# Kernel tuning notes

Hardware: AMD Instinct MI355X
Metric: run time of the kernel (lower is better)

The kernel has to match this reference:

```python
import jax, jax.numpy as jnp
import numpy as np

WD, WH, WW = 1, 8, 8           # window size
NH = 2                          # num heads
EPS = 1e-5                      # torch LayerNorm default


def _layernorm(x, g, b):
    mu = jnp.mean(x, axis=-1, keepdims=True)
    var = jnp.mean((x - mu) ** 2, axis=-1, keepdims=True)
    return (x - mu) * jax.lax.rsqrt(var + EPS) * g + b


def setup_inputs() -> dict:
    key = jax.random.key(0)
    ks = jax.random.split(key, 12)
    C, H = 192, 768  # dim, mlp hidden
    w = lambda k, shape: (jax.random.normal(k, shape, jnp.float32) * 0.02)
    return {
        "x": jax.random.normal(ks[0], (2, 8, 96, 96, C), jnp.float32),
        "norm3_g": jnp.ones((C,), jnp.float32),
        "norm3_b": jnp.zeros((C,), jnp.float32),
        "in_proj_w": w(ks[1], (3 * C, C)),
        "in_proj_b": jnp.zeros((3 * C,), jnp.float32),
        "out_proj_w": w(ks[2], (C, C)),
        "out_proj_b": jnp.zeros((C,), jnp.float32),
        "norm4_g": jnp.ones((C,), jnp.float32),
        "norm4_b": jnp.zeros((C,), jnp.float32),
        "fc1_w": w(ks[3], (H, C)),
        "fc1_b": jnp.zeros((H,), jnp.float32),
        "fc2_w": w(ks[4], (C, H)),
        "fc2_b": jnp.zeros((C,), jnp.float32),
    }


def _part3(x, norm3_g, norm3_b, in_proj_w, in_proj_b, out_proj_w, out_proj_b):
    B, D, H, W, C = x.shape
    Dn, Hn, Wn = D // WD, H // WH, W // WW
    P = Hn * Wn          # spatial windows
    Wt = WD * WH * WW    # tokens per window (64)
    L = Dn * Wt          # attention sequence length

    xn = _layernorm(x, norm3_g, norm3_b)
    # window partition: (B, Dn, Hn, Wn, wd, wh, ww, C)
    xw = xn.reshape(B, Dn, WD, Hn, WH, Wn, WW, C).transpose(0, 1, 3, 5, 2, 4, 6, 7)
    # tgt: (B, Dn, P, Wt, C) -> h: (B*P, Dn*Wt, C)
    tgt = xw.reshape(B, Dn, P, Wt, C)
    h = tgt.transpose(0, 2, 1, 3, 4).reshape(B * P, L, C)

    # qkv projection (torch Linear convention: x @ W.T + b)
    qkv = h @ in_proj_w.T + in_proj_b          # (Bp, L, 3C)
    q, k, v = jnp.split(qkv, 3, axis=-1)
    hd = C // NH
    q = q.reshape(B * P, L, NH, hd)
    k = k.reshape(B * P, L, NH, hd)
    v = v.reshape(B * P, L, NH, hd)

    # block-causal mask over temporal index (each block is Wt x Wt)
    neg_inf = jnp.finfo(jnp.float32).min
    tmask = jnp.triu(jnp.full((Dn, Dn), neg_inf, jnp.float32), k=1)
    mask = jnp.repeat(jnp.repeat(tmask, Wt, axis=0), Wt, axis=1)  # (L, L)

    scale = 1.0 / np.sqrt(hd)
    scores = jnp.einsum("blhd,bmhd->bhlm", q * scale, k) + mask
    attn = jax.nn.softmax(scores, axis=-1)
    out = jnp.einsum("bhlm,bmhd->blhd", attn, v).reshape(B * P, L, C)
    out = out @ out_proj_w.T + out_proj_b

    # reverse: (B, P, Dn, Wt, C) -> windows -> (B, D, H, W, C)
    out = out.reshape(B, P, Dn, Wt, C).transpose(0, 2, 1, 3, 4)
    out = out.reshape(B, Dn, Hn, Wn, WD, WH, WW, C)
    out = out.transpose(0, 1, 4, 2, 5, 3, 6, 7).reshape(B, D, H, W, C)
    return out


def reference(x, norm3_g, norm3_b, in_proj_w, in_proj_b, out_proj_w, out_proj_b,
              norm4_g, norm4_b, fc1_w, fc1_b, fc2_w, fc2_b):
    x = x + _part3(x, norm3_g, norm3_b, in_proj_w, in_proj_b, out_proj_w, out_proj_b)
    xn = _layernorm(x, norm4_g, norm4_b)
    mlp = jax.nn.gelu(xn @ fc1_w.T + fc1_b, approximate=False) @ fc2_w.T + fc2_b
    return x + mlp
```

## Files before the change

### kernel.cpp

```cpp
#include <hip/hip_runtime.h>
#include <cstdint>
#include <cstddef>


typedef float   f32x4  __attribute__((ext_vector_type(4)));
typedef __bf16  bf16x8 __attribute__((ext_vector_type(8)));
typedef unsigned int   u32x4  __attribute__((ext_vector_type(4)));
typedef unsigned short u16x4  __attribute__((ext_vector_type(4)));

#define DEVI __device__ __forceinline__

DEVI float bf2f(unsigned short u) {
    union { unsigned int i; float f; } v; v.i = ((unsigned int)u) << 16; return v.f;
}
DEVI unsigned short f2bf(float f) {
    unsigned int u = __builtin_bit_cast(unsigned int, f);
    unsigned int r = u + 0x7fffu + ((u >> 16) & 1u);
    return (unsigned short)(r >> 16);
}

typedef __attribute__((address_space(3))) unsigned char       lds_u8;
typedef __attribute__((address_space(1))) const unsigned char g_u8;
DEVI void gl_lds16(const void* g, void* l) {
    __builtin_amdgcn_global_load_lds((g_u8*)g, (lds_u8*)l, 16, 0, 0);
}

__global__ __launch_bounds__(256) void k_wconv(const float* __restrict__ wqkv,
                                               const float* __restrict__ wout,
                                               const float* __restrict__ wfc1,
                                               const float* __restrict__ wfc2,
                                               unsigned short* __restrict__ oq,
                                               unsigned short* __restrict__ oo,
                                               unsigned short* __restrict__ o1,
                                               unsigned short* __restrict__ o2) {
    int i = blockIdx.x * 256 + threadIdx.x;
    if (i < 122880) {
        int r = i / 192;
        oq[i] = (r < 576) ? f2bf(wqkv[i]) : (unsigned short)0;
    } else if (i < 172032) {
        int j = i - 122880; int r = j / 192;
        oo[j] = (r < 192) ? f2bf(wout[j]) : (unsigned short)0;
    } else if (i < 319488) {
        int j = i - 172032;
        o1[j] = f2bf(wfc1[j]);
    } else if (i < 516096) {
        int j = i - 319488; int r = j / 768;
        o2[j] = (r < 192) ? f2bf(wfc2[j]) : (unsigned short)0;
    }
}

__global__ __launch_bounds__(256) void k_ln3(const float* __restrict__ x,
                                             const float* __restrict__ g,
                                             const float* __restrict__ bsh,
                                             unsigned short* __restrict__ h) {
    int w = threadIdx.x >> 6, lane = threadIdx.x & 63;
    int token = blockIdx.x * 4 + w;
    const float* xp = x + (size_t)token * 192;
    float v0 = xp[lane], v1 = xp[lane + 64], v2 = xp[lane + 128];
    float s = v0 + v1 + v2;
#pragma unroll
    for (int off = 32; off; off >>= 1) s += __shfl_xor(s, off);
    float mean = s * (1.f / 192.f);
    float d0 = v0 - mean, d1 = v1 - mean, d2 = v2 - mean;
    float q = d0 * d0 + d1 * d1 + d2 * d2;
#pragma unroll
    for (int off = 32; off; off >>= 1) q += __shfl_xor(q, off);
    float rs = rsqrtf(q * (1.f / 192.f) + 1e-5f);
    int b  = token / (8 * 96 * 96);
    int r0 = token - b * (8 * 96 * 96);
    int d  = r0 / (96 * 96);
    int r1 = r0 - d * (96 * 96);
    int hh = r1 / 96;
    int ww = r1 - hh * 96;
    int bp = b * 144 + (hh >> 3) * 12 + (ww >> 3);
    int l  = d * 64 + (hh & 7) * 8 + (ww & 7);
    unsigned short* hp = h + ((size_t)bp * 512 + l) * 192;
    hp[lane]       = f2bf(d0 * rs * g[lane]       + bsh[lane]);
    hp[lane + 64]  = f2bf(d1 * rs * g[lane + 64]  + bsh[lane + 64]);
    hp[lane + 128] = f2bf(d2 * rs * g[lane + 128] + bsh[lane + 128]);
}

__global__ __launch_bounds__(256) void k_ln4b(const unsigned short* __restrict__ yb,
                                              const float* __restrict__ g,
                                              const float* __restrict__ bsh,
                                              unsigned short* __restrict__ xn) {
    int sub = threadIdx.x >> 5, tl = threadIdx.x & 31;
    size_t row = (size_t)blockIdx.x * 8 + sub;
    const unsigned int* rp = reinterpret_cast<const unsigned int*>(yb + row * 192);
    float v[6];
#pragma unroll
    for (int j = 0; j < 3; j++) {
        unsigned int w = rp[tl + 32 * j];
        v[2 * j]     = bf2f((unsigned short)(w & 0xffffu));
        v[2 * j + 1] = bf2f((unsigned short)(w >> 16));
    }
    float s = v[0] + v[1] + v[2] + v[3] + v[4] + v[5];
#pragma unroll
    for (int off = 1; off < 32; off <<= 1) s += __shfl_xor(s, off);
    float mean = s * (1.f / 192.f);
    float q = 0.f;
#pragma unroll
    for (int j = 0; j < 6; j++) { v[j] -= mean; q += v[j] * v[j]; }
#pragma unroll
    for (int off = 1; off < 32; off <<= 1) q += __shfl_xor(q, off);
    float rs = rsqrtf(q * (1.f / 192.f) + 1e-5f);
    unsigned int* op = reinterpret_cast<unsigned int*>(xn + row * 192);
#pragma unroll
    for (int j = 0; j < 3; j++) {
        int c = (tl + 32 * j) * 2;
        unsigned short lo = f2bf(v[2 * j]     * rs * g[c]     + bsh[c]);
        unsigned short hi = f2bf(v[2 * j + 1] * rs * g[c + 1] + bsh[c + 1]);
        op[tl + 32 * j] = ((unsigned int)hi << 16) | lo;
    }
}

template <int EPI, int K>
__global__ __launch_bounds__(256) void k_gemm128(const unsigned short* __restrict__ A,
                                                 const unsigned short* __restrict__ Bw,
                                                 const float* __restrict__ bias,
                                                 unsigned short* __restrict__ outb,
                                                 unsigned short* __restrict__ vt,
                                                 float* __restrict__ outf,
                                                 const float* __restrict__ res,
                                                 const unsigned short* __restrict__ resb) {
    __shared__ unsigned short As[2][128 * 64];
    __shared__ unsigned short Bs[2][128 * 64];
    const int tid = threadIdx.x;
    const int nwg = gridDim.x * gridDim.y;
    const int flat = blockIdx.y * gridDim.x + blockIdx.x;
    const int swz = (flat & 7) * (nwg >> 3) + (flat >> 3);
    const int bx = swz % gridDim.x, by = swz / gridDim.x;
    const int row0 = by * 128, col0 = bx * 128;
    const int wv = tid >> 6, lane = tid & 63, lr = lane & 15, lg = lane >> 4;
    const int wr = wv >> 1, wc = wv & 1;
    const int sr = lane >> 3, sc = lane & 7;
    f32x4 acc[4][4] = {};

    auto stage = [&](int t, int buf) {
        int k0 = t * 64;
#pragma unroll
        for (int i = 0; i < 4; i++) {
            int gq = wv * 4 + i;
            int r = gq * 8 + sr;
            int j = sc ^ (r & 7);
            gl_lds16(A + (size_t)(row0 + r) * K + k0 + j * 8, &As[buf][gq * 512]);
        }
#pragma unroll
        for (int i = 0; i < 4; i++) {
            int gq = wv * 4 + i;
            int r = gq * 8 + sr;
            int j = sc ^ (r & 7);
            gl_lds16(Bw + (size_t)(col0 + r) * K + k0 + j * 8, &Bs[buf][gq * 512]);
        }
    };

    const int NT = K / 64;
    stage(0, 0);
    for (int t = 0; t < NT; ++t) {
        int cur = t & 1;
        if (t + 1 < NT) {
            stage(t + 1, cur ^ 1);
            asm volatile("s_waitcnt vmcnt(8)" ::: "memory");
        } else {
            asm volatile("s_waitcnt vmcnt(0)" ::: "memory");
        }
        __builtin_amdgcn_sched_barrier(0);
        __builtin_amdgcn_s_barrier();
        __builtin_amdgcn_sched_barrier(0);
#pragma unroll
        for (int kk = 0; kk < 64; kk += 32) {
            bf16x8 af[4], bf[4];
#pragma unroll
            for (int m = 0; m < 4; m++) {
                int r = wr * 64 + m * 16 + lr;
                int j = ((kk >> 3) + lg) ^ (r & 7);
                af[m] = __builtin_bit_cast(bf16x8,
                    *reinterpret_cast<const u32x4*>(&As[cur][r * 64 + j * 8]));
            }
#pragma unroll
            for (int n = 0; n < 4; n++) {
                int r = wc * 64 + n * 16 + lr;
                int j = ((kk >> 3) + lg) ^ (r & 7);
                bf[n] = __builtin_bit_cast(bf16x8,
                    *reinterpret_cast<const u32x4*>(&Bs[cur][r * 64 + j * 8]));
            }
#pragma unroll
            for (int m = 0; m < 4; m++)
#pragma unroll
                for (int n = 0; n < 4; n++)
                    acc[m][n] = __builtin_amdgcn_mfma_f32_16x16x32_bf16(af[m], bf[n], acc[m][n], 0, 0, 0);
        }
        __builtin_amdgcn_sched_barrier(0);
        __builtin_amdgcn_s_barrier();
        __builtin_amdgcn_sched_barrier(0);
    }

#pragma unroll
    for (int m = 0; m < 4; m++) {
#pragma unroll
        for (int n = 0; n < 4; n++) {
            int col  = col0 + wc * 64 + n * 16 + lr;
            int rowb = row0 + wr * 64 + m * 16 + lg * 4;
            if constexpr (EPI == 0) {
                if (col < 384) {
                    float b = bias[col];
                    float sc2 = (col < 192) ? 0.1020620726159658f : 1.f;
#pragma unroll
                    for (int rr = 0; rr < 4; rr++)
                        outb[(size_t)(rowb + rr) * 384 + col] = f2bf((acc[m][n][rr] + b) * sc2);
                } else if (col < 576) {
                    float b = bias[col];
                    int head = (col >= 480) ? 1 : 0;
                    int d = col - 384 - head * 96;
                    int bp = rowb >> 9, tok = rowb & 511;
                    u16x4 pk = { f2bf(acc[m][n][0] + b), f2bf(acc[m][n][1] + b),
                                 f2bf(acc[m][n][2] + b), f2bf(acc[m][n][3] + b) };
                    *reinterpret_cast<u16x4*>(vt + ((size_t)(bp * 2 + head) * 96 + d) * 512 + tok) = pk;
                }
            } else if constexpr (EPI == 1) {
                if (col < 192) {
                    float b = bias[col];
#pragma unroll
                    for (int rr = 0; rr < 4; rr++) {
                        int nrow = rowb + rr;
                        int bp = nrow >> 9, l = nrow & 511;
                        int bb = bp / 144, p = bp - bb * 144;
                        int hn = p / 12, wn = p - hn * 12;
                        int dn = l >> 6, t_ = l & 63;
                        size_t tok = ((size_t)((bb * 8 + dn) * 96 + hn * 8 + (t_ >> 3)) * 96 + wn * 8 + (t_ & 7));
                        size_t idx = tok * 192 + col;
                        outb[idx] = f2bf(res[idx] + acc[m][n][rr] + b);
                    }
                }
            } else if constexpr (EPI == 2) {
                float b = bias[col];
#pragma unroll
                for (int rr = 0; rr < 4; rr++) {
                    float v = acc[m][n][rr] + b;
                    float gz = 0.5f * v * (1.f + erff(v * 0.70710678118654752f));
                    outb[(size_t)(rowb + rr) * 768 + col] = f2bf(gz);
                }
            } else {
                if (col < 192) {
                    float b = bias[col];
#pragma unroll
                    for (int rr = 0; rr < 4; rr++) {
                        size_t idx = (size_t)(rowb + rr) * 192 + col;
                        outf[idx] = bf2f(resb[idx]) + acc[m][n][rr] + b;
                    }
                }
            }
        }
    }
}

__global__ __launch_bounds__(512) void k_attn(const unsigned short* __restrict__ qk,
                                              const unsigned short* __restrict__ vt,
                                              unsigned short* __restrict__ aout) {
    __shared__ unsigned short Ks[64][104];
    __shared__ unsigned short Vs[96][72];
    __shared__ unsigned short Ps[8][16][72];

    int bid = (blockIdx.x & 7) * 288 + (blockIdx.x >> 3);
    int bp = bid >> 3, rest = bid & 7, head = rest >> 2, pr = rest & 3;
    int tid = threadIdx.x, wv = tid >> 6, lane = tid & 63;
    int lr = lane & 15, lg = lane >> 4;
    int wq = wv & 3, wt = wv >> 2;
    int nk = 2 * pr + 2;

    size_t qrow0 = (size_t)bp * 512 + (size_t)(2 * pr + wt) * 64;
    const unsigned short* vbase = vt + (size_t)(bp * 2 + head) * 96 * 512;
    size_t krowb = (size_t)bp * 512;

    bf16x8 qf[3];
    {
        const unsigned short* qp = qk + (qrow0 + wq * 16 + lr) * 384 + head * 96 + lg * 8;
#pragma unroll
        for (int ks = 0; ks < 3; ks++)
            qf[ks] = __builtin_bit_cast(bf16x8, *reinterpret_cast<const u32x4*>(qp + ks * 32));
    }

    f32x4 o[6] = {};
    float m_ = -1e30f, lsum = 0.f;

    u32x4 sreg[3];
    auto issue = [&](int dnk) {
#pragma unroll
        for (int i = 0; i < 3; i++) {
            int c = tid + i * 512;
            if (c < 768) {
                int r = c / 12, cc = c - r * 12;
                sreg[i] = *reinterpret_cast<const u32x4*>(
                    qk + (krowb + dnk * 64 + r) * 384 + 192 + head * 96 + cc * 8);
            } else {
                int c2 = c - 768; int d = c2 >> 3, tb = c2 & 7;
                sreg[i] = *reinterpret_cast<const u32x4*>(
                    vbase + (size_t)d * 512 + dnk * 64 + tb * 8);
            }
        }
    };
    auto commit = [&]() {
#pragma unroll
        for (int i = 0; i < 3; i++) {
            int c = tid + i * 512;
            if (c < 768) {
                int r = c / 12, cc = c - r * 12;
                *reinterpret_cast<u32x4*>(&Ks[r][cc * 8]) = sreg[i];
            } else {
                int c2 = c - 768; int d = c2 >> 3, tb = c2 & 7;
                *reinterpret_cast<u32x4*>(&Vs[d][tb * 8]) = sreg[i];
            }
        }
    };

    issue(0);
    for (int dnk = 0; dnk < nk; ++dnk) {
        commit();
        __syncthreads();
        if (dnk + 1 < nk) issue(dnk + 1);
        if (wt == 1 || dnk < nk - 1) {
            f32x4 st[4] = {};
#pragma unroll
            for (int ks = 0; ks < 3; ks++) {
#pragma unroll
                for (int ct = 0; ct < 4; ct++) {
                    bf16x8 kf = __builtin_bit_cast(bf16x8,
                        *reinterpret_cast<const u32x4*>(&Ks[ct * 16 + lr][ks * 32 + lg * 8]));
                    st[ct] = __builtin_amdgcn_mfma_f32_16x16x32_bf16(kf, qf[ks], st[ct], 0, 0, 0);
                }
            }
            float mx = st[0][0];
#pragma unroll
            for (int ct = 0; ct < 4; ct++)
#pragma unroll
                for (int rr = 0; rr < 4; rr++) mx = fmaxf(mx, st[ct][rr]);
            mx = fmaxf(mx, __shfl_xor(mx, 16));
            mx = fmaxf(mx, __shfl_xor(mx, 32));
            float mnew = fmaxf(m_, mx);
            float corr = __expf(m_ - mnew);
            m_ = mnew;
            float ps = 0.f;
#pragma unroll
            for (int ct = 0; ct < 4; ct++) {
                u16x4 pk;
#pragma unroll
                for (int rr = 0; rr < 4; rr++) {
                    float pv = __expf(st[ct][rr] - mnew);
                    ps += pv;
                    pk[rr] = f2bf(pv);
                }
                *reinterpret_cast<u16x4*>(&Ps[wv][lr][ct * 16 + lg * 4]) = pk;
            }
            ps += __shfl_xor(ps, 16);
            ps += __shfl_xor(ps, 32);
            lsum = lsum * corr + ps;
#pragma unroll
            for (int rr = 0; rr < 4; rr++) {
                float cr = __shfl(corr, (lane & 48) | (lg * 4 + rr));
#pragma unroll
                for (int nf = 0; nf < 6; nf++) o[nf][rr] *= cr;
            }
#pragma unroll
            for (int kk = 0; kk < 2; kk++) {
                bf16x8 pf = __builtin_bit_cast(bf16x8,
                    *reinterpret_cast<const u32x4*>(&Ps[wv][lr][kk * 32 + lg * 8]));
#pragma unroll
                for (int nf = 0; nf < 6; nf++) {
                    bf16x8 vf = __builtin_bit_cast(bf16x8,
                        *reinterpret_cast<const u32x4*>(&Vs[nf * 16 + lr][kk * 32 + lg * 8]));
                    o[nf] = __builtin_amdgcn_mfma_f32_16x16x32_bf16(pf, vf, o[nf], 0, 0, 0);
                }
            }
        }
        __syncthreads();
    }

#pragma unroll
    for (int rr = 0; rr < 4; rr++) {
        float li = __shfl(lsum, (lane & 48) | (lg * 4 + rr));
        float inv = 1.f / li;
        size_t row = qrow0 + wq * 16 + lg * 4 + rr;
#pragma unroll
        for (int nf = 0; nf < 6; nf++)
            aout[row * 192 + head * 96 + nf * 16 + lr] = f2bf(o[nf][rr] * inv);
    }
}

extern "C" void kernel_launch(void* const* d_in, const int* in_sizes, int n_in,
                              void* d_out, int out_size, void* d_ws, size_t ws_size,
                              hipStream_t stream) {
    const float* x    = (const float*)d_in[0];
    const float* n3g  = (const float*)d_in[1];
    const float* n3b  = (const float*)d_in[2];
    const float* wqkv = (const float*)d_in[3];
    const float* bqkv = (const float*)d_in[4];
    const float* wout = (const float*)d_in[5];
    const float* bout = (const float*)d_in[6];
    const float* n4g  = (const float*)d_in[7];
    const float* n4b  = (const float*)d_in[8];
    const float* wfc1 = (const float*)d_in[9];
    const float* bfc1 = (const float*)d_in[10];
    const float* wfc2 = (const float*)d_in[11];
    const float* bfc2 = (const float*)d_in[12];
    float* out = (float*)d_out;

    char* ws = (char*)d_ws;
    unsigned short* qk     = (unsigned short*)(ws + 0);
    unsigned short* vt     = (unsigned short*)(ws + 113246208);
    unsigned short* h      = (unsigned short*)(ws + 169869312);
    unsigned short* attn   = (unsigned short*)(ws + 226492416);
    unsigned short* xn4    = (unsigned short*)(ws + 226492416);
    unsigned short* hidden = (unsigned short*)(ws + 0);
    unsigned short* wq_bf  = (unsigned short*)(ws + 283115520);
    unsigned short* wo_bf  = (unsigned short*)(ws + 283361280);
    unsigned short* w1_bf  = (unsigned short*)(ws + 283459584);
    unsigned short* w2_bf  = (unsigned short*)(ws + 283754496);
    unsigned short* ybf    = (unsigned short*)(ws + 284147712);

    k_wconv<<<2016, 256, 0, stream>>>(wqkv, wout, wfc1, wfc2, wq_bf, wo_bf, w1_bf, w2_bf);
    k_ln3<<<36864, 256, 0, stream>>>(x, n3g, n3b, h);
    k_gemm128<0, 192><<<dim3(5, 1152), 256, 0, stream>>>(h, wq_bf, bqkv, qk, vt, nullptr, nullptr, nullptr);
    k_attn<<<2304, 512, 0, stream>>>(qk, vt, attn);
    k_gemm128<1, 192><<<dim3(2, 1152), 256, 0, stream>>>(attn, wo_bf, bout, ybf, nullptr, nullptr, x, nullptr);
    k_ln4b<<<18432, 256, 0, stream>>>(ybf, n4g, n4b, xn4);
    k_gemm128<2, 192><<<dim3(6, 1152), 256, 0, stream>>>(xn4, w1_bf, bfc1, hidden, nullptr, nullptr, nullptr, nullptr);
    k_gemm128<3, 768><<<dim3(2, 1152), 256, 0, stream>>>(hidden, w2_bf, bfc2, nullptr, nullptr, out, nullptr, ybf);
}
```

Before: 587.1 us.

## Transpose MFMA output for vectorized epilogues, use tanh GELU, widen fc2 tile

```diff
diff --git a/kernel.cpp b/kernel.cpp
--- a/kernel.cpp
+++ b/kernel.cpp
@@ -17,6 +17,13 @@
     unsigned int u = __builtin_bit_cast(unsigned int, f);
     unsigned int r = u + 0x7fffu + ((u >> 16) & 1u);
     return (unsigned short)(r >> 16);
+}
+DEVI float gelu_fast(float v) {
+    float t = v * v;
+    float z = v * (1.5957691216057308f + 0.07135481627f * t);
+    float e = __expf(z);
+    float r = 2.0f / (1.0f + e);
+    return v - 0.5f * v * r;
 }
 
 typedef __attribute__((address_space(3))) unsigned char       lds_u8;
@@ -114,7 +121,7 @@
     }
 }
 
-template <int EPI, int K>
+template <int EPI, int K, int NF>
 __global__ __launch_bounds__(256) void k_gemm128(const unsigned short* __restrict__ A,
                                                  const unsigned short* __restrict__ Bw,
                                                  const float* __restrict__ bias,
@@ -123,18 +130,19 @@
                                                  float* __restrict__ outf,
                                                  const float* __restrict__ res,
                                                  const unsigned short* __restrict__ resb) {
+    constexpr int BN = NF * 32;
     __shared__ unsigned short As[2][128 * 64];
-    __shared__ unsigned short Bs[2][128 * 64];
+    __shared__ unsigned short Bs[2][BN * 64];
     const int tid = threadIdx.x;
     const int nwg = gridDim.x * gridDim.y;
     const int flat = blockIdx.y * gridDim.x + blockIdx.x;
     const int swz = (flat & 7) * (nwg >> 3) + (flat >> 3);
     const int bx = swz % gridDim.x, by = swz / gridDim.x;
-    const int row0 = by * 128, col0 = bx * 128;
+    const int row0 = by * 128, col0 = bx * BN;
     const int wv = tid >> 6, lane = tid & 63, lr = lane & 15, lg = lane >> 4;
     const int wr = wv >> 1, wc = wv & 1;
     const int sr = lane >> 3, sc = lane & 7;
-    f32x4 acc[4][4] = {};
+    f32x4 acc[4][NF] = {};
 
     auto stage = [&](int t, int buf) {
         int k0 = t * 64;
@@ -146,8 +154,8 @@
             gl_lds16(A + (size_t)(row0 + r) * K + k0 + j * 8, &As[buf][gq * 512]);
         }
 #pragma unroll
-        for (int i = 0; i < 4; i++) {
-            int gq = wv * 4 + i;
+        for (int i = 0; i < NF; i++) {
+            int gq = wv * NF + i;
             int r = gq * 8 + sr;
             int j = sc ^ (r & 7);
             gl_lds16(Bw + (size_t)(col0 + r) * K + k0 + j * 8, &Bs[buf][gq * 512]);
@@ -160,7 +168,8 @@
         int cur = t & 1;
         if (t + 1 < NT) {
             stage(t + 1, cur ^ 1);
-            asm volatile("s_waitcnt vmcnt(8)" ::: "memory");
+            if constexpr (NF == 4) asm volatile("s_waitcnt vmcnt(8)" ::: "memory");
+            else                   asm volatile("s_waitcnt vmcnt(10)" ::: "memory");
         } else {
             asm volatile("s_waitcnt vmcnt(0)" ::: "memory");
         }
@@ -169,7 +178,7 @@
         __builtin_amdgcn_sched_barrier(0);
 #pragma unroll
         for (int kk = 0; kk < 64; kk += 32) {
-            bf16x8 af[4], bf[4];
+            bf16x8 af[4], bf[NF];
 #pragma unroll
             for (int m = 0; m < 4; m++) {
                 int r = wr * 64 + m * 16 + lr;
@@ -178,8 +187,8 @@
                     *reinterpret_cast<const u32x4*>(&As[cur][r * 64 + j * 8]));
             }
 #pragma unroll
-            for (int n = 0; n < 4; n++) {
-                int r = wc * 64 + n * 16 + lr;
+            for (int n = 0; n < NF; n++) {
+                int r = wc * (NF * 16) + n * 16 + lr;
                 int j = ((kk >> 3) + lg) ^ (r & 7);
                 bf[n] = __builtin_bit_cast(bf16x8,
                     *reinterpret_cast<const u32x4*>(&Bs[cur][r * 64 + j * 8]));
@@ -187,8 +196,8 @@
 #pragma unroll
             for (int m = 0; m < 4; m++)
 #pragma unroll
-                for (int n = 0; n < 4; n++)
-                    acc[m][n] = __builtin_amdgcn_mfma_f32_16x16x32_bf16(af[m], bf[n], acc[m][n], 0, 0, 0);
+                for (int n = 0; n < NF; n++)
+                    acc[m][n] = __builtin_amdgcn_mfma_f32_16x16x32_bf16(bf[n], af[m], acc[m][n], 0, 0, 0);
         }
         __builtin_amdgcn_sched_barrier(0);
         __builtin_amdgcn_s_barrier();
@@ -197,58 +206,54 @@
 
 #pragma unroll
     for (int m = 0; m < 4; m++) {
-#pragma unroll
-        for (int n = 0; n < 4; n++) {
-            int col  = col0 + wc * 64 + n * 16 + lr;
-            int rowb = row0 + wr * 64 + m * 16 + lg * 4;
+        const int arow = row0 + wr * 64 + m * 16 + lr;
+#pragma unroll
+        for (int n = 0; n < NF; n++) {
+            const int colb = col0 + wc * (NF * 16) + n * 16 + lg * 4;
             if constexpr (EPI == 0) {
-                if (col < 384) {
-                    float b = bias[col];
-                    float sc2 = (col < 192) ? 0.1020620726159658f : 1.f;
+                if (colb < 384) {
+                    f32x4 b4 = *reinterpret_cast<const f32x4*>(bias + colb);
+                    float sc2 = (colb < 192) ? 0.1020620726159658f : 1.f;
+                    u16x4 pk;
+#pragma unroll
+                    for (int rr = 0; rr < 4; rr++) pk[rr] = f2bf((acc[m][n][rr] + b4[rr]) * sc2);
+                    *reinterpret_cast<u16x4*>(outb + (size_t)arow * 384 + colb) = pk;
+                } else if (colb < 576) {
+                    int head = (colb >= 480) ? 1 : 0;
+                    int bp = arow >> 9, tok = arow & 511;
+                    size_t vb = ((size_t)(bp * 2 + head) * 96 + (colb - 384 - head * 96)) * 512 + tok;
 #pragma unroll
                     for (int rr = 0; rr < 4; rr++)
-                        outb[(size_t)(rowb + rr) * 384 + col] = f2bf((acc[m][n][rr] + b) * sc2);
-                } else if (col < 576) {
-                    float b = bias[col];
-                    int head = (col >= 480) ? 1 : 0;
-                    int d = col - 384 - head * 96;
-                    int bp = rowb >> 9, tok = rowb & 511;
-                    u16x4 pk = { f2bf(acc[m][n][0] + b), f2bf(acc[m][n][1] + b),
-                                 f2bf(acc[m][n][2] + b), f2bf(acc[m][n][3] + b) };
-                    *reinterpret_cast<u16x4*>(vt + ((size_t)(bp * 2 + head) * 96 + d) * 512 + tok) = pk;
+                        vt[vb + (size_t)rr * 512] = f2bf(acc[m][n][rr] + bias[colb + rr]);
                 }
             } else if constexpr (EPI == 1) {
-                if (col < 192) {
-                    float b = bias[col];
-#pragma unroll
-                    for (int rr = 0; rr < 4; rr++) {
-                        int nrow = rowb + rr;
-                        int bp = nrow >> 9, l = nrow & 511;
-                        int bb = bp / 144, p = bp - bb * 144;
-                        int hn = p / 12, wn = p - hn * 12;
-                        int dn = l >> 6, t_ = l & 63;
-                        size_t tok = ((size_t)((bb * 8 + dn) * 96 + hn * 8 + (t_ >> 3)) * 96 + wn * 8 + (t_ & 7));
-                        size_t idx = tok * 192 + col;
-                        outb[idx] = f2bf(res[idx] + acc[m][n][rr] + b);
-                    }
+                if (colb < 192) {
+                    int bp = arow >> 9, l = arow & 511;
+                    int bb = bp / 144, p = bp - bb * 144;
+                    int hn = p / 12, wn = p - hn * 12;
+                    int dn = l >> 6, t_ = l & 63;
+                    size_t tok = ((size_t)((bb * 8 + dn) * 96 + hn * 8 + (t_ >> 3)) * 96 + wn * 8 + (t_ & 7));
+                    size_t idx = tok * 192 + colb;
+                    f32x4 r4 = *reinterpret_cast<const f32x4*>(res + idx);
+                    f32x4 b4 = *reinterpret_cast<const f32x4*>(bias + colb);
+                    u16x4 pk;
+#pragma unroll
+                    for (int rr = 0; rr < 4; rr++) pk[rr] = f2bf(r4[rr] + acc[m][n][rr] + b4[rr]);
+                    *reinterpret_cast<u16x4*>(outb + idx) = pk;
                 }
             } else if constexpr (EPI == 2) {
-                float b = bias[col];
-#pragma unroll
-                for (int rr = 0; rr < 4; rr++) {
-                    float v = acc[m][n][rr] + b;
-                    float gz = 0.5f * v * (1.f + erff(v * 0.70710678118654752f));
-                    outb[(size_t)(rowb + rr) * 768 + col] = f2bf(gz);
-                }
+                f32x4 b4 = *reinterpret_cast<const f32x4*>(bias + colb);
+                u16x4 pk;
+#pragma unroll
+                for (int rr = 0; rr < 4; rr++) pk[rr] = f2bf(gelu_fast(acc[m][n][rr] + b4[rr]));
+                *reinterpret_cast<u16x4*>(outb + (size_t)arow * 768 + colb) = pk;
             } else {
-                if (col < 192) {
-                    float b = bias[col];
-#pragma unroll
-                    for (int rr = 0; rr < 4; rr++) {
-                        size_t idx = (size_t)(rowb + rr) * 192 + col;
-                        outf[idx] = bf2f(resb[idx]) + acc[m][n][rr] + b;
-                    }
-                }
+                f32x4 b4 = *reinterpret_cast<const f32x4*>(bias + colb);
+                u16x4 rb = *reinterpret_cast<const u16x4*>(resb + (size_t)arow * 192 + colb);
+                f32x4 o4;
+#pragma unroll
+                for (int rr = 0; rr < 4; rr++) o4[rr] = bf2f(rb[rr]) + acc[m][n][rr] + b4[rr];
+                *reinterpret_cast<f32x4*>(outf + (size_t)arow * 192 + colb) = o4;
             }
         }
     }
@@ -419,10 +424,10 @@
 
     k_wconv<<<2016, 256, 0, stream>>>(wqkv, wout, wfc1, wfc2, wq_bf, wo_bf, w1_bf, w2_bf);
     k_ln3<<<36864, 256, 0, stream>>>(x, n3g, n3b, h);
-    k_gemm128<0, 192><<<dim3(5, 1152), 256, 0, stream>>>(h, wq_bf, bqkv, qk, vt, nullptr, nullptr, nullptr);
+    k_gemm128<0, 192, 4><<<dim3(5, 1152), 256, 0, stream>>>(h, wq_bf, bqkv, qk, vt, nullptr, nullptr, nullptr);
     k_attn<<<2304, 512, 0, stream>>>(qk, vt, attn);
-    k_gemm128<1, 192><<<dim3(2, 1152), 256, 0, stream>>>(attn, wo_bf, bout, ybf, nullptr, nullptr, x, nullptr);
+    k_gemm128<1, 192, 4><<<dim3(2, 1152), 256, 0, stream>>>(attn, wo_bf, bout, ybf, nullptr, nullptr, x, nullptr);
     k_ln4b<<<18432, 256, 0, stream>>>(ybf, n4g, n4b, xn4);
-    k_gemm128<2, 192><<<dim3(6, 1152), 256, 0, stream>>>(xn4, w1_bf, bfc1, hidden, nullptr, nullptr, nullptr, nullptr);
-    k_gemm128<3, 768><<<dim3(2, 1152), 256, 0, stream>>>(hidden, w2_bf, bfc2, nullptr, nullptr, out, nullptr, ybf);
-}
+    k_gemm128<2, 192, 4><<<dim3(6, 1152), 256, 0, stream>>>(xn4, w1_bf, bfc1, hidden, nullptr, nullptr, nullptr, nullptr);
+    k_gemm128<3, 768, 6><<<dim3(1, 1152), 256, 0, stream>>>(hidden, w2_bf, bfc2, nullptr, nullptr, out, nullptr, ybf);
+}
```

Result: slower. 600.5 us (+2.3%).
